# Performance work log

Hardware: AMD Instinct MI355X
Metric: run time of the kernel (lower is better)

Reference implementation:

```python
import jax, jax.numpy as jnp
import numpy as np

K = 1024      # size_codebook
D = 64        # dim_codebook
N = 131072    # number of input vectors
GAMMA = 0.99
ALPHA = 1e-09
BETA = 0.25


def setup_inputs() -> dict:
    key = jax.random.key(0)
    k1, k2, k3 = jax.random.split(key, 3)
    X = jax.random.normal(k1, (N, D), dtype=jnp.float32)
    E = jax.random.normal(k2, (K, D), dtype=jnp.float32)
    cluster_sizes = jnp.zeros((K,), dtype=jnp.float32)
    moving_avg = E  # buffer initialized to a clone of E.weight
    return {"X": X, "E": E, "cluster_sizes": cluster_sizes, "moving_avg": moving_avg}


def reference(X, E, cluster_sizes, moving_avg):
    # squared euclidean distances: [N, K]
    X_sqnorm = jnp.sum(X * X, axis=1, keepdims=True)          # [N, 1]
    E_sqnorm = jnp.sum(E * E, axis=1)[None, :]                # [1, K]
    dist = X_sqnorm + E_sqnorm - 2.0 * (X @ E.T)              # [N, K]
    min_dist = jnp.min(dist, axis=1)                          # [N]
    argmins = jnp.argmin(dist, axis=1)                        # [N]
    Z_embs_raw = E[argmins]                                   # [N, D]

    # commitment loss (codebook is detached in the EMA variant)
    diff = X - jax.lax.stop_gradient(Z_embs_raw)
    loss = BETA * jnp.mean(jnp.sum(diff * diff, axis=1))

    # EMA codebook update (training mode, no-grad in torch)
    counts = jax.ops.segment_sum(jnp.ones((N,), dtype=X.dtype), argmins, num_segments=K)
    cs = GAMMA * cluster_sizes + (1.0 - GAMMA) * counts
    cs = (cs + ALPHA) / (1.0 + ALPHA * K / jnp.sum(cs))
    sums = jax.ops.segment_sum(X, argmins, num_segments=K)    # one_hot.T @ X, [K, D]
    ma = GAMMA * moving_avg + (1.0 - GAMMA) * sums
    E_new = ma / cs[:, None]

    # straight-through estimator
    Z_embs = X + jax.lax.stop_gradient(Z_embs_raw - X)
    return (Z_embs, loss, argmins, min_dist, E_new, cs, ma)
```

## Files before the change

### kernel.cpp

```cpp
#include <hip/hip_runtime.h>
#include <math.h>

#define NN 131072
#define KK 1024
#define DD 64
#define GAMMA 0.99f
#define ALPHA 1e-9f
#define BETA 0.25f

typedef float f32x4 __attribute__((ext_vector_type(4)));
typedef short bf16x8 __attribute__((ext_vector_type(8)));

__device__ __constant__ float OMG = (float)(1.0 - 0.99);

__device__ __forceinline__ void split_bf16(float v, unsigned short& h, unsigned short& l) {
    unsigned int b = __float_as_uint(v);
    unsigned int hb = b & 0xFFFF0000u;
    h = (unsigned short)(hb >> 16);
    float r = v - __uint_as_float(hb);
    unsigned int lb = __float_as_uint(r);
    lb += 0x7FFFu + ((lb >> 16) & 1u);
    l = (unsigned short)(lb >> 16);
}

__global__ __launch_bounds__(64)
void vq_prep(const float* __restrict__ E, float4* __restrict__ Efrag,
             float* __restrict__ esq) {
    int nt = blockIdx.x;
    int l = threadIdx.x;
    int n = nt * 16 + (l & 15);
    int kb = (l >> 4) * 8;
    float ss = 0.f;
    #pragma unroll
    for (int ks = 0; ks < 2; ++ks) {
        const float4* xp = (const float4*)(E + (size_t)n * DD + ks * 32 + kb);
        float4 a = xp[0], b = xp[1];
        float v[8] = {a.x, a.y, a.z, a.w, b.x, b.y, b.z, b.w};
        union { float4 f; unsigned short u[8]; } H, L;
        #pragma unroll
        for (int j = 0; j < 8; ++j) {
            unsigned short hh, ll;
            split_bf16(v[j], hh, ll);
            H.u[j] = hh; L.u[j] = ll;
            ss = fmaf(v[j], v[j], ss);
        }
        int fid = nt * 4 + ks * 2;
        Efrag[(size_t)(fid + 0) * 64 + l] = H.f;
        Efrag[(size_t)(fid + 1) * 64 + l] = L.f;
    }
    ss += __shfl_xor(ss, 16, 64);
    ss += __shfl_xor(ss, 32, 64);
    if (l < 16) esq[nt * 16 + l] = ss;
}

#define BM 128

__global__ __launch_bounds__(256, 2)
void vq_main(const float* __restrict__ X, const float* __restrict__ E,
             const float4* __restrict__ Efrag, const float* __restrict__ esq,
             float* __restrict__ argf, float* __restrict__ mind,
             float* __restrict__ Z, int* __restrict__ cursor,
             int* __restrict__ rowlist, float* __restrict__ sumsFB,
             float* __restrict__ loss_part, int cap) {
    __shared__ float redv[256];
    __shared__ int redi[256];
    __shared__ int bidx[128];
    __shared__ float bsc[128];
    __shared__ float xsqs[128];
    __shared__ int fbflag[128];

    int tid = threadIdx.x;
    int lane = tid & 63, w = tid >> 6;
    int rg = w & 1, cg = w >> 1;
    int lc = lane & 15, lq = lane >> 4;

    size_t bb = (size_t)blockIdx.x * BM;
    size_t R0 = bb + rg * 64;

    bf16x8 ah[4][2], al[4][2];
    #pragma unroll
    for (int mt = 0; mt < 4; ++mt) {
        float xq = 0.f;
        #pragma unroll
        for (int ks = 0; ks < 2; ++ks) {
            const float4* xp =
                (const float4*)(X + (R0 + mt * 16 + lc) * DD + ks * 32 + lq * 8);
            float4 x0 = xp[0], x1 = xp[1];
            float v[8] = {x0.x, x0.y, x0.z, x0.w, x1.x, x1.y, x1.z, x1.w};
            union { bf16x8 s; unsigned short u[8]; } H, L;
            #pragma unroll
            for (int j = 0; j < 8; ++j) {
                unsigned short hh, ll;
                split_bf16(v[j], hh, ll);
                H.u[j] = hh; L.u[j] = ll;
                xq = fmaf(v[j], v[j], xq);
            }
            ah[mt][ks] = H.s;
            al[mt][ks] = L.s;
        }
        xq += __shfl_xor(xq, 16, 64);
        xq += __shfl_xor(xq, 32, 64);
        if (lane < 16) xsqs[rg * 64 + mt * 16 + lane] = xq;
    }

    float bestv[4][4];
    int besti[4][4];
    #pragma unroll
    for (int mt = 0; mt < 4; ++mt)
        #pragma unroll
        for (int r = 0; r < 4; ++r) { bestv[mt][r] = 3.402823466e38f; besti[mt][r] = 0; }

    const float4* bp = Efrag + (size_t)(cg * 32) * 256 + lane;
    const float* ep = esq + cg * 512 + lc;

    float4 nb0 = bp[0], nb1 = bp[64], nb2 = bp[128], nb3 = bp[192];
    float en = ep[0];

    for (int nt = 0; nt < 32; ++nt) {
        float4 cb0 = nb0, cb1 = nb1, cb2 = nb2, cb3 = nb3;
        float ec = en;
        if (nt < 31) {
            const float4* q = bp + (size_t)(nt + 1) * 256;
            nb0 = q[0]; nb1 = q[64]; nb2 = q[128]; nb3 = q[192];
            en = ep[(nt + 1) * 16];
        }
        union { float4 f; bf16x8 s; } u0, u1, u2, u3;
        u0.f = cb0; u1.f = cb1; u2.f = cb2; u3.f = cb3;
        bf16x8 bh0 = u0.s, bl0 = u1.s, bh1 = u2.s, bl1 = u3.s;

        f32x4 acc[4];
        #pragma unroll
        for (int mt = 0; mt < 4; ++mt) acc[mt] = (f32x4){0.f, 0.f, 0.f, 0.f};

        #pragma unroll
        for (int mt = 0; mt < 4; ++mt)
            acc[mt] = __builtin_amdgcn_mfma_f32_16x16x32_bf16(ah[mt][0], bh0, acc[mt], 0, 0, 0);
        #pragma unroll
        for (int mt = 0; mt < 4; ++mt)
            acc[mt] = __builtin_amdgcn_mfma_f32_16x16x32_bf16(ah[mt][1], bh1, acc[mt], 0, 0, 0);
        #pragma unroll
        for (int mt = 0; mt < 4; ++mt)
            acc[mt] = __builtin_amdgcn_mfma_f32_16x16x32_bf16(ah[mt][0], bl0, acc[mt], 0, 0, 0);
        #pragma unroll
        for (int mt = 0; mt < 4; ++mt)
            acc[mt] = __builtin_amdgcn_mfma_f32_16x16x32_bf16(ah[mt][1], bl1, acc[mt], 0, 0, 0);
        #pragma unroll
        for (int mt = 0; mt < 4; ++mt)
            acc[mt] = __builtin_amdgcn_mfma_f32_16x16x32_bf16(al[mt][0], bh0, acc[mt], 0, 0, 0);
        #pragma unroll
        for (int mt = 0; mt < 4; ++mt)
            acc[mt] = __builtin_amdgcn_mfma_f32_16x16x32_bf16(al[mt][1], bh1, acc[mt], 0, 0, 0);

        int n = cg * 512 + nt * 16 + lc;
        #pragma unroll
        for (int mt = 0; mt < 4; ++mt) {
            #pragma unroll
            for (int r = 0; r < 4; ++r) {
                float sc = fmaf(-2.f, acc[mt][r], ec);
                if (sc < bestv[mt][r]) { bestv[mt][r] = sc; besti[mt][r] = n; }
            }
        }
    }

    #pragma unroll
    for (int off = 1; off <= 8; off <<= 1) {
        #pragma unroll
        for (int mt = 0; mt < 4; ++mt) {
            #pragma unroll
            for (int r = 0; r < 4; ++r) {
                float ov = __shfl_xor(bestv[mt][r], off, 64);
                int oi = __shfl_xor(besti[mt][r], off, 64);
                if (ov < bestv[mt][r] || (ov == bestv[mt][r] && oi < besti[mt][r])) {
                    bestv[mt][r] = ov; besti[mt][r] = oi;
                }
            }
        }
    }
    if (lc == 0) {
        #pragma unroll
        for (int mt = 0; mt < 4; ++mt)
            #pragma unroll
            for (int r = 0; r < 4; ++r) {
                int row = rg * 64 + mt * 16 + lq * 4 + r;
                redv[row * 2 + cg] = bestv[mt][r];
                redi[row * 2 + cg] = besti[mt][r];
            }
    }
    __syncthreads();
    if (tid < 128) {
        float v0 = redv[tid * 2], v1 = redv[tid * 2 + 1];
        int i0 = redi[tid * 2], i1 = redi[tid * 2 + 1];
        int pick = (v1 < v0 || (v1 == v0 && i1 < i0));
        bidx[tid] = pick ? i1 : i0;
        bsc[tid] = pick ? v1 : v0;
    }
    __syncthreads();

    float md = 0.f;
    if (lane < 32) {
        int row = w * 32 + lane;
        int bi = bidx[row];
        size_t grow = bb + row;
        md = xsqs[row] + bsc[row];
        mind[grow] = md;
        argf[grow] = (float)bi;
        int pos = atomicAdd(&cursor[bi], 1);
        if (pos < cap) {
            rowlist[(size_t)bi * cap + pos] = (int)grow;
            fbflag[row] = 0;
        } else {
            fbflag[row] = 1;
        }
    }
    #pragma unroll
    for (int m = 32; m; m >>= 1) md += __shfl_xor(md, m, 64);
    if (lane == 0) atomicAdd(&loss_part[(blockIdx.x * 4 + w) & 1023], md);
    __syncthreads();

    for (int it = 0; it < 32; ++it) {
        int row = w * 32 + it;
        int bi = bidx[row];
        size_t grow = bb + row;
        float e = E[(size_t)bi * DD + lane];
        Z[grow * DD + lane] = e;
        if (fbflag[row]) {
            float x = X[grow * DD + lane];
            atomicAdd(&sumsFB[(size_t)bi * DD + lane], x);
        }
    }
}

__global__ __launch_bounds__(1024)
void vq_cs(const float* __restrict__ cluster_sizes, const int* __restrict__ cursor,
           const float* __restrict__ loss_part, float* __restrict__ out_cs,
           float* __restrict__ out_loss) {
    __shared__ float red[1024];
    int k = threadIdx.x;
    float csr = GAMMA * cluster_sizes[k] + OMG * (float)cursor[k];
    red[k] = csr;
    __syncthreads();
    for (int off = 512; off; off >>= 1) {
        if (k < off) red[k] += red[k + off];
        __syncthreads();
    }
    float total = red[0];
    __syncthreads();
    red[k] = loss_part[k];
    __syncthreads();
    for (int off = 512; off; off >>= 1) {
        if (k < off) red[k] += red[k + off];
        __syncthreads();
    }
    if (k == 0) out_loss[0] = BETA * (red[0] / (float)NN);

    float denom = 1.0f + (ALPHA * (float)KK) / total;
    out_cs[k] = (csr + ALPHA) / denom;
}

__global__ __launch_bounds__(256)
void vq_sum_ema(const float* __restrict__ X, const int* __restrict__ rowlist,
                const int* __restrict__ cursor, const float* __restrict__ sumsFB,
                const float* __restrict__ cs, const float* __restrict__ mavg,
                float* __restrict__ o_ma, float* __restrict__ o_enew, int cap) {
    __shared__ float part[4][64];
    int k = blockIdx.x;
    int lane = threadIdx.x & 63, w = threadIdx.x >> 6;
    int cnt = cursor[k];
    int nr = cnt < cap ? cnt : cap;
    const int* rl = rowlist + (size_t)k * cap;
    float acc = 0.f;
    #pragma unroll 4
    for (int i = w; i < nr; i += 4) {
        int r = rl[i];
        acc += X[(size_t)r * DD + lane];
    }
    part[w][lane] = acc;
    __syncthreads();
    if (w == 0) {
        float s = part[0][lane] + part[1][lane] + part[2][lane] + part[3][lane]
                + sumsFB[(size_t)k * DD + lane];
        float ma = GAMMA * mavg[(size_t)k * DD + lane] + OMG * s;
        o_ma[(size_t)k * DD + lane] = ma;
        o_enew[(size_t)k * DD + lane] = ma / cs[k];
    }
}

extern "C" void kernel_launch(void* const* d_in, const int* in_sizes, int n_in,
                              void* d_out, int out_size, void* d_ws, size_t ws_size,
                              hipStream_t stream) {
    const float* X = (const float*)d_in[0];
    const float* E = (const float*)d_in[1];
    const float* cluster_sizes = (const float*)d_in[2];
    const float* moving_avg = (const float*)d_in[3];

    float* out = (float*)d_out;
    float* o_Z = out;
    float* o_loss = o_Z + (size_t)NN * DD;
    float* o_arg = o_loss + 1;
    float* o_mind = o_arg + NN;
    float* o_enew = o_mind + NN;
    float* o_cs = o_enew + (size_t)KK * DD;
    float* o_ma = o_cs + KK;

    int* cursor = (int*)d_ws;
    float* loss_part = (float*)d_ws + 1024;
    float* sumsFB = loss_part + 1024;
    float* esq = sumsFB + (size_t)KK * DD;
    float4* Efrag = (float4*)(esq + KK);
    int* rowlist = (int*)(esq + KK + (size_t)KK * DD);

    size_t base_bytes = (size_t)(1024 + 1024 + KK * DD + KK + KK * DD) * 4;
    long cap_l = ((long)ws_size - (long)base_bytes) / (long)(KK * sizeof(int));
    int cap = cap_l < 0 ? 0 : (cap_l > 1024 ? 1024 : (int)cap_l);

    hipMemsetAsync(d_ws, 0, (size_t)(1024 + 1024 + KK * DD) * 4, stream);

    vq_prep<<<KK / 16, 64, 0, stream>>>(E, Efrag, esq);
    vq_main<<<NN / BM, 256, 0, stream>>>(X, E, Efrag, esq, o_arg, o_mind, o_Z,
                                         cursor, rowlist, sumsFB, loss_part, cap);
    vq_cs<<<1, 1024, 0, stream>>>(cluster_sizes, cursor, loss_part, o_cs, o_loss);
    vq_sum_ema<<<KK, 256, 0, stream>>>(X, rowlist, cursor, sumsFB, o_cs,
                                       moving_avg, o_ma, o_enew, cap);
}
```

Before: 241.3 us.

## Halve row tile, fold norm into MFMA accumulator, merge cs kernel into EMA

The row tile per block drops from 128 to 64, giving twice as many blocks and fewer live accumulator registers per wave. The codebook norm is stored pre-scaled by -0.5 and used as the MFMA accumulator's initial value, so the argmin becomes an argmax on the raw accumulator and the per-element fma goes away. The single-block vq_cs kernel is removed: each vq_sum_ema block recomputes the cluster-size total redundantly, and block 0 also reduces the loss. The trade-offs are fewer MFMA tiles reusing each codebook fragment load and duplicated reduction work in every EMA block.

New measurement: 230.2 us. -4.6%, faster.

```diff
diff --git a/kernel.cpp b/kernel.cpp
--- a/kernel.cpp
+++ b/kernel.cpp
@@ -25,7 +25,7 @@
 
 __global__ __launch_bounds__(64)
 void vq_prep(const float* __restrict__ E, float4* __restrict__ Efrag,
-             float* __restrict__ esq) {
+             float* __restrict__ esqh) {
     int nt = blockIdx.x;
     int l = threadIdx.x;
     int n = nt * 16 + (l & 15);
@@ -50,24 +50,24 @@
     }
     ss += __shfl_xor(ss, 16, 64);
     ss += __shfl_xor(ss, 32, 64);
-    if (l < 16) esq[nt * 16 + l] = ss;
-}
-
-#define BM 128
+    if (l < 16) esqh[nt * 16 + l] = -0.5f * ss;
+}
+
+#define BM 64
 
 __global__ __launch_bounds__(256, 2)
 void vq_main(const float* __restrict__ X, const float* __restrict__ E,
-             const float4* __restrict__ Efrag, const float* __restrict__ esq,
+             const float4* __restrict__ Efrag, const float* __restrict__ esqh,
              float* __restrict__ argf, float* __restrict__ mind,
              float* __restrict__ Z, int* __restrict__ cursor,
              int* __restrict__ rowlist, float* __restrict__ sumsFB,
              float* __restrict__ loss_part, int cap) {
-    __shared__ float redv[256];
-    __shared__ int redi[256];
-    __shared__ int bidx[128];
-    __shared__ float bsc[128];
-    __shared__ float xsqs[128];
-    __shared__ int fbflag[128];
+    __shared__ float redv[128];
+    __shared__ int redi[128];
+    __shared__ int bidx[64];
+    __shared__ float bsc[64];
+    __shared__ float xsqs[64];
+    __shared__ int fbflag[64];
 
     int tid = threadIdx.x;
     int lane = tid & 63, w = tid >> 6;
@@ -75,11 +75,11 @@
     int lc = lane & 15, lq = lane >> 4;
 
     size_t bb = (size_t)blockIdx.x * BM;
-    size_t R0 = bb + rg * 64;
-
-    bf16x8 ah[4][2], al[4][2];
-    #pragma unroll
-    for (int mt = 0; mt < 4; ++mt) {
+    size_t R0 = bb + rg * 32;
+
+    bf16x8 ah[2][2], al[2][2];
+    #pragma unroll
+    for (int mt = 0; mt < 2; ++mt) {
         float xq = 0.f;
         #pragma unroll
         for (int ks = 0; ks < 2; ++ks) {
@@ -100,18 +100,18 @@
         }
         xq += __shfl_xor(xq, 16, 64);
         xq += __shfl_xor(xq, 32, 64);
-        if (lane < 16) xsqs[rg * 64 + mt * 16 + lane] = xq;
-    }
-
-    float bestv[4][4];
-    int besti[4][4];
-    #pragma unroll
-    for (int mt = 0; mt < 4; ++mt)
-        #pragma unroll
-        for (int r = 0; r < 4; ++r) { bestv[mt][r] = 3.402823466e38f; besti[mt][r] = 0; }
+        if (lane < 16) xsqs[rg * 32 + mt * 16 + lane] = xq;
+    }
+
+    float bestv[2][4];
+    int besti[2][4];
+    #pragma unroll
+    for (int mt = 0; mt < 2; ++mt)
+        #pragma unroll
+        for (int r = 0; r < 4; ++r) { bestv[mt][r] = -3.402823466e38f; besti[mt][r] = 0; }
 
     const float4* bp = Efrag + (size_t)(cg * 32) * 256 + lane;
-    const float* ep = esq + cg * 512 + lc;
+    const float* ep = esqh + cg * 512 + lc;
 
     float4 nb0 = bp[0], nb1 = bp[64], nb2 = bp[128], nb3 = bp[192];
     float en = ep[0];
@@ -128,36 +128,36 @@
         u0.f = cb0; u1.f = cb1; u2.f = cb2; u3.f = cb3;
         bf16x8 bh0 = u0.s, bl0 = u1.s, bh1 = u2.s, bl1 = u3.s;
 
-        f32x4 acc[4];
-        #pragma unroll
-        for (int mt = 0; mt < 4; ++mt) acc[mt] = (f32x4){0.f, 0.f, 0.f, 0.f};
-
-        #pragma unroll
-        for (int mt = 0; mt < 4; ++mt)
+        f32x4 acc[2];
+        #pragma unroll
+        for (int mt = 0; mt < 2; ++mt) acc[mt] = (f32x4){ec, ec, ec, ec};
+
+        #pragma unroll
+        for (int mt = 0; mt < 2; ++mt)
             acc[mt] = __builtin_amdgcn_mfma_f32_16x16x32_bf16(ah[mt][0], bh0, acc[mt], 0, 0, 0);
         #pragma unroll
-        for (int mt = 0; mt < 4; ++mt)
+        for (int mt = 0; mt < 2; ++mt)
             acc[mt] = __builtin_amdgcn_mfma_f32_16x16x32_bf16(ah[mt][1], bh1, acc[mt], 0, 0, 0);
         #pragma unroll
-        for (int mt = 0; mt < 4; ++mt)
+        for (int mt = 0; mt < 2; ++mt)
             acc[mt] = __builtin_amdgcn_mfma_f32_16x16x32_bf16(ah[mt][0], bl0, acc[mt], 0, 0, 0);
         #pragma unroll
-        for (int mt = 0; mt < 4; ++mt)
+        for (int mt = 0; mt < 2; ++mt)
             acc[mt] = __builtin_amdgcn_mfma_f32_16x16x32_bf16(ah[mt][1], bl1, acc[mt], 0, 0, 0);
         #pragma unroll
-        for (int mt = 0; mt < 4; ++mt)
+        for (int mt = 0; mt < 2; ++mt)
             acc[mt] = __builtin_amdgcn_mfma_f32_16x16x32_bf16(al[mt][0], bh0, acc[mt], 0, 0, 0);
         #pragma unroll
-        for (int mt = 0; mt < 4; ++mt)
+        for (int mt = 0; mt < 2; ++mt)
             acc[mt] = __builtin_amdgcn_mfma_f32_16x16x32_bf16(al[mt][1], bh1, acc[mt], 0, 0, 0);
 
         int n = cg * 512 + nt * 16 + lc;
         #pragma unroll
-        for (int mt = 0; mt < 4; ++mt) {
+        for (int mt = 0; mt < 2; ++mt) {
             #pragma unroll
             for (int r = 0; r < 4; ++r) {
-                float sc = fmaf(-2.f, acc[mt][r], ec);
-                if (sc < bestv[mt][r]) { bestv[mt][r] = sc; besti[mt][r] = n; }
+                float sc = acc[mt][r];
+                if (sc > bestv[mt][r]) { bestv[mt][r] = sc; besti[mt][r] = n; }
             }
         }
     }
@@ -165,12 +165,12 @@
     #pragma unroll
     for (int off = 1; off <= 8; off <<= 1) {
         #pragma unroll
-        for (int mt = 0; mt < 4; ++mt) {
+        for (int mt = 0; mt < 2; ++mt) {
             #pragma unroll
             for (int r = 0; r < 4; ++r) {
                 float ov = __shfl_xor(bestv[mt][r], off, 64);
                 int oi = __shfl_xor(besti[mt][r], off, 64);
-                if (ov < bestv[mt][r] || (ov == bestv[mt][r] && oi < besti[mt][r])) {
+                if (ov > bestv[mt][r] || (ov == bestv[mt][r] && oi < besti[mt][r])) {
                     bestv[mt][r] = ov; besti[mt][r] = oi;
                 }
             }
@@ -178,30 +178,29 @@
     }
     if (lc == 0) {
         #pragma unroll
-        for (int mt = 0; mt < 4; ++mt)
+        for (int mt = 0; mt < 2; ++mt)
             #pragma unroll
             for (int r = 0; r < 4; ++r) {
-                int row = rg * 64 + mt * 16 + lq * 4 + r;
+                int row = rg * 32 + mt * 16 + lq * 4 + r;
                 redv[row * 2 + cg] = bestv[mt][r];
                 redi[row * 2 + cg] = besti[mt][r];
             }
     }
     __syncthreads();
-    if (tid < 128) {
+    if (tid < 64) {
         float v0 = redv[tid * 2], v1 = redv[tid * 2 + 1];
         int i0 = redi[tid * 2], i1 = redi[tid * 2 + 1];
-        int pick = (v1 < v0 || (v1 == v0 && i1 < i0));
+        int pick = (v1 > v0 || (v1 == v0 && i1 < i0));
         bidx[tid] = pick ? i1 : i0;
         bsc[tid] = pick ? v1 : v0;
     }
     __syncthreads();
 
-    float md = 0.f;
-    if (lane < 32) {
-        int row = w * 32 + lane;
+    if (tid < 64) {
+        int row = tid;
         int bi = bidx[row];
         size_t grow = bb + row;
-        md = xsqs[row] + bsc[row];
+        float md = fmaf(-2.f, bsc[row], xsqs[row]);
         mind[grow] = md;
         argf[grow] = (float)bi;
         int pos = atomicAdd(&cursor[bi], 1);
@@ -211,14 +210,15 @@
         } else {
             fbflag[row] = 1;
         }
-    }
-    #pragma unroll
-    for (int m = 32; m; m >>= 1) md += __shfl_xor(md, m, 64);
-    if (lane == 0) atomicAdd(&loss_part[(blockIdx.x * 4 + w) & 1023], md);
-    __syncthreads();
-
-    for (int it = 0; it < 32; ++it) {
-        int row = w * 32 + it;
+        #pragma unroll
+        for (int m = 32; m; m >>= 1) md += __shfl_xor(md, m, 64);
+        if (tid == 0) atomicAdd(&loss_part[blockIdx.x & 1023], md);
+    }
+    __syncthreads();
+
+    #pragma unroll 4
+    for (int it = 0; it < 16; ++it) {
+        int row = w * 16 + it;
         int bi = bidx[row];
         size_t grow = bb + row;
         float e = E[(size_t)bi * DD + lane];
@@ -230,41 +230,44 @@
     }
 }
 
-__global__ __launch_bounds__(1024)
-void vq_cs(const float* __restrict__ cluster_sizes, const int* __restrict__ cursor,
-           const float* __restrict__ loss_part, float* __restrict__ out_cs,
-           float* __restrict__ out_loss) {
-    __shared__ float red[1024];
-    int k = threadIdx.x;
-    float csr = GAMMA * cluster_sizes[k] + OMG * (float)cursor[k];
-    red[k] = csr;
-    __syncthreads();
-    for (int off = 512; off; off >>= 1) {
-        if (k < off) red[k] += red[k + off];
-        __syncthreads();
-    }
-    float total = red[0];
-    __syncthreads();
-    red[k] = loss_part[k];
-    __syncthreads();
-    for (int off = 512; off; off >>= 1) {
-        if (k < off) red[k] += red[k + off];
-        __syncthreads();
-    }
-    if (k == 0) out_loss[0] = BETA * (red[0] / (float)NN);
-
-    float denom = 1.0f + (ALPHA * (float)KK) / total;
-    out_cs[k] = (csr + ALPHA) / denom;
-}
-
 __global__ __launch_bounds__(256)
 void vq_sum_ema(const float* __restrict__ X, const int* __restrict__ rowlist,
                 const int* __restrict__ cursor, const float* __restrict__ sumsFB,
-                const float* __restrict__ cs, const float* __restrict__ mavg,
-                float* __restrict__ o_ma, float* __restrict__ o_enew, int cap) {
+                const float* __restrict__ cluster_sizes,
+                const float* __restrict__ loss_part, const float* __restrict__ mavg,
+                float* __restrict__ o_ma, float* __restrict__ o_enew,
+                float* __restrict__ o_cs, float* __restrict__ o_loss, int cap) {
     __shared__ float part[4][64];
+    __shared__ float redt[4];
     int k = blockIdx.x;
     int lane = threadIdx.x & 63, w = threadIdx.x >> 6;
+
+    float t = 0.f;
+    for (int j = threadIdx.x; j < KK; j += 256)
+        t += GAMMA * cluster_sizes[j] + OMG * (float)cursor[j];
+    #pragma unroll
+    for (int m = 32; m; m >>= 1) t += __shfl_xor(t, m, 64);
+    if (lane == 0) redt[w] = t;
+    __syncthreads();
+    float total = redt[0] + redt[1] + redt[2] + redt[3];
+
+    float csr = GAMMA * cluster_sizes[k] + OMG * (float)cursor[k];
+    float cs = (csr + ALPHA) / (1.0f + (ALPHA * (float)KK) / total);
+    if (threadIdx.x == 0) o_cs[k] = cs;
+
+    if (k == 0) {
+        float t2 = 0.f;
+        for (int j = threadIdx.x; j < 1024; j += 256) t2 += loss_part[j];
+        #pragma unroll
+        for (int m = 32; m; m >>= 1) t2 += __shfl_xor(t2, m, 64);
+        if (lane == 0) redt[w] = t2;
+        __syncthreads();
+        if (threadIdx.x == 0) {
+            float l = redt[0] + redt[1] + redt[2] + redt[3];
+            o_loss[0] = BETA * (l / (float)NN);
+        }
+    }
+
     int cnt = cursor[k];
     int nr = cnt < cap ? cnt : cap;
     const int* rl = rowlist + (size_t)k * cap;
@@ -281,7 +284,7 @@
                 + sumsFB[(size_t)k * DD + lane];
         float ma = GAMMA * mavg[(size_t)k * DD + lane] + OMG * s;
         o_ma[(size_t)k * DD + lane] = ma;
-        o_enew[(size_t)k * DD + lane] = ma / cs[k];
+        o_enew[(size_t)k * DD + lane] = ma / cs;
     }
 }
 
@@ -305,9 +308,9 @@
     int* cursor = (int*)d_ws;
     float* loss_part = (float*)d_ws + 1024;
     float* sumsFB = loss_part + 1024;
-    float* esq = sumsFB + (size_t)KK * DD;
-    float4* Efrag = (float4*)(esq + KK);
-    int* rowlist = (int*)(esq + KK + (size_t)KK * DD);
+    float* esqh = sumsFB + (size_t)KK * DD;
+    float4* Efrag = (float4*)(esqh + KK);
+    int* rowlist = (int*)(esqh + KK + (size_t)KK * DD);
 
     size_t base_bytes = (size_t)(1024 + 1024 + KK * DD + KK + KK * DD) * 4;
     long cap_l = ((long)ws_size - (long)base_bytes) / (long)(KK * sizeof(int));
@@ -315,10 +318,10 @@
 
     hipMemsetAsync(d_ws, 0, (size_t)(1024 + 1024 + KK * DD) * 4, stream);
 
-    vq_prep<<<KK / 16, 64, 0, stream>>>(E, Efrag, esq);
-    vq_main<<<NN / BM, 256, 0, stream>>>(X, E, Efrag, esq, o_arg, o_mind, o_Z,
+    vq_prep<<<KK / 16, 64, 0, stream>>>(E, Efrag, esqh);
+    vq_main<<<NN / BM, 256, 0, stream>>>(X, E, Efrag, esqh, o_arg, o_mind, o_Z,
                                          cursor, rowlist, sumsFB, loss_part, cap);
-    vq_cs<<<1, 1024, 0, stream>>>(cluster_sizes, cursor, loss_part, o_cs, o_loss);
-    vq_sum_ema<<<KK, 256, 0, stream>>>(X, rowlist, cursor, sumsFB, o_cs,
-                                       moving_avg, o_ma, o_enew, cap);
-}
+    vq_sum_ema<<<KK, 256, 0, stream>>>(X, rowlist, cursor, sumsFB, cluster_sizes,
+                                       loss_part, moving_avg, o_ma, o_enew,
+                                       o_cs, o_loss, cap);
+}
```
